# Kernel optimization log

Measured on AMD Instinct MI355X. Metric: run time of the kernel, lower is better.

Reference implementation:

```python
import jax, jax.numpy as jnp
import numpy as np
import math

IN_DIM = 512
OUT_DIM = 512
MOD_DIM = 512
B, S = 4, 4096
EPS = 1e-8


def setup_inputs() -> dict:
    key = jax.random.key(0)
    k1, k2, k3, k4 = jax.random.split(key, 4)
    x = jax.random.normal(k1, (B, S, IN_DIM), dtype=jnp.float32)
    modulation = jax.random.normal(k2, (B, S, MOD_DIM), dtype=jnp.float32)
    # main weight: kaiming_normal_(a=0.2, fan_in, leaky_relu) -> std = sqrt(2/(1+0.2^2)) / sqrt(in_dim)
    gain = math.sqrt(2.0 / (1.0 + 0.2 ** 2))
    weight = gain / math.sqrt(IN_DIM) * jax.random.normal(k3, (OUT_DIM, IN_DIM), dtype=jnp.float32)
    bias = jnp.zeros((OUT_DIM,), dtype=jnp.float32)
    # modulation Linear: cips_bias_init -> weight ~ N(0, 1/sqrt(fan_in)), bias = 1.0
    mod_w = (1.0 / math.sqrt(MOD_DIM)) * jax.random.normal(k4, (IN_DIM, MOD_DIM), dtype=jnp.float32)
    mod_b = jnp.ones((IN_DIM,), dtype=jnp.float32)
    return {"x": x, "modulation": modulation, "weight": weight, "bias": bias,
            "mod_w": mod_w, "mod_b": mod_b}


def reference(x, modulation, weight, bias, mod_w, mod_b):
    # s = modulation linear -> per-token scale on input features  [B,S,in]
    s = jnp.einsum('bsm,im->bsi', modulation, mod_w) + mod_b
    # Algebraic rewrite of StyleGAN2 modulated linear (same math, never
    # materializes [B,S,out,in]):
    #   out[b,s,o] = sum_i (W[o,i]*s[b,s,i]*demod[b,s,o]) * x[b,s,i]
    #             = demod[b,s,o] * sum_i W[o,i] * (s*x)[b,s,i]
    #   demod = rsqrt(sum_i (W[o,i]*s[b,s,i])^2 + eps)
    out = jnp.einsum('bsi,oi->bso', x * s, weight)
    demod = jax.lax.rsqrt(jnp.einsum('bsi,oi->bso', s * s, weight * weight) + EPS)
    # torch computes demod under no_grad -> constant; irrelevant for fwd but kept explicit
    out = out * jax.lax.stop_gradient(demod) + bias
    return out
```

## Files before the change

### kernel.cpp

```cpp
#include <hip/hip_runtime.h>
#include <hip/hip_bf16.h>


#define T_TOK 16384
#define DIM 512

typedef __attribute__((ext_vector_type(4))) float f32x4;
typedef __attribute__((ext_vector_type(8))) short bf16x8;

static __device__ __forceinline__ unsigned short f2bf(float f) {
    union { float f; unsigned int u; } v; v.f = f;
    unsigned int u = v.u;
    u += 0x7fffu + ((u >> 16) & 1u);
    return (unsigned short)(u >> 16);
}
static __device__ __forceinline__ float bf2f(unsigned short h) {
    union { unsigned int u; float f; } v; v.u = ((unsigned int)h) << 16;
    return v.f;
}

__global__ __launch_bounds__(256) void k0_convert(
    const float* __restrict__ mod, const float* __restrict__ weight,
    const float* __restrict__ mod_w,
    unsigned short* __restrict__ modb, unsigned short* __restrict__ Wb,
    unsigned short* __restrict__ W2b, unsigned short* __restrict__ mwb)
{
    const int NV_MOD = (T_TOK * DIM) / 4;
    const int NV_W   = (DIM * DIM) / 4;
    int idx = blockIdx.x * blockDim.x + threadIdx.x;
    int stride = gridDim.x * blockDim.x;
    for (int i = idx; i < NV_MOD; i += stride) {
        f32x4 v = ((const f32x4*)mod)[i];
        ushort4 o; o.x = f2bf(v[0]); o.y = f2bf(v[1]); o.z = f2bf(v[2]); o.w = f2bf(v[3]);
        ((ushort4*)modb)[i] = o;
    }
    for (int i = idx; i < NV_W; i += stride) {
        f32x4 v = ((const f32x4*)weight)[i];
        ushort4 o;  o.x = f2bf(v[0]); o.y = f2bf(v[1]); o.z = f2bf(v[2]); o.w = f2bf(v[3]);
        ((ushort4*)Wb)[i] = o;
        ushort4 o2; o2.x = f2bf(v[0]*v[0]); o2.y = f2bf(v[1]*v[1]);
                    o2.z = f2bf(v[2]*v[2]); o2.w = f2bf(v[3]*v[3]);
        ((ushort4*)W2b)[i] = o2;
        f32x4 m = ((const f32x4*)mod_w)[i];
        ushort4 o3; o3.x = f2bf(m[0]); o3.y = f2bf(m[1]); o3.z = f2bf(m[2]); o3.w = f2bf(m[3]);
        ((ushort4*)mwb)[i] = o3;
    }
}


__global__ __launch_bounds__(256, 2) void k1_style(
    const unsigned short* __restrict__ modb,
    const unsigned short* __restrict__ mwb,
    const float* __restrict__ x,
    const float* __restrict__ mod_b,
    unsigned short* __restrict__ xs,
    unsigned short* __restrict__ ss)
{
    __shared__ union {
        struct { unsigned short A[128 * 64]; unsigned short B[128 * 64]; } stg;
        unsigned short str[128 * 144];
    } u;
    const int tid  = threadIdx.x;
    const int lane = tid & 63;
    const int w    = tid >> 6;
    const int wr   = w >> 1, wc = w & 1;
    const int nbn  = DIM / 128;
    const int bm   = blockIdx.x / nbn;
    const int bn   = blockIdx.x % nbn;

    const int srow  = lane >> 3;
    const int lslot = (lane & 7) ^ srow;
    const int fr    = lane & 15;
    const int fs    = lane >> 4;

    f32x4 acc[4][4] = {};

    const size_t aBase = (size_t)bm * 128 * DIM;
    const size_t bBase = (size_t)bn * 128 * DIM;

    for (int kb = 0; kb < DIM; kb += 64) {
#pragma unroll
        for (int q = 0; q < 4; ++q) {
            int row = w * 32 + q * 8 + srow;
            const unsigned short* ga = modb + aBase + (size_t)row * DIM + kb + lslot * 8;
            const unsigned short* gb = mwb  + bBase + (size_t)row * DIM + kb + lslot * 8;
            __builtin_amdgcn_global_load_lds(
                (__attribute__((address_space(1))) void*)ga,
                (__attribute__((address_space(3))) void*)(u.stg.A + w * 2048 + q * 512), 16, 0, 0);
            __builtin_amdgcn_global_load_lds(
                (__attribute__((address_space(1))) void*)gb,
                (__attribute__((address_space(3))) void*)(u.stg.B + w * 2048 + q * 512), 16, 0, 0);
        }
        __syncthreads();
#pragma unroll
        for (int kk = 0; kk < 64; kk += 32) {
            bf16x8 af[4], bfv[4];
#pragma unroll
            for (int mi = 0; mi < 4; ++mi) {
                int row = wr * 64 + mi * 16 + fr;
                int ps  = ((kk >> 3) + fs) ^ (fr & 7);
                af[mi] = *(const bf16x8*)(u.stg.A + row * 64 + ps * 8);
            }
#pragma unroll
            for (int ni = 0; ni < 4; ++ni) {
                int row = wc * 64 + ni * 16 + fr;
                int ps  = ((kk >> 3) + fs) ^ (fr & 7);
                bfv[ni] = *(const bf16x8*)(u.stg.B + row * 64 + ps * 8);
            }
#pragma unroll
            for (int mi = 0; mi < 4; ++mi)
#pragma unroll
                for (int ni = 0; ni < 4; ++ni)
                    acc[mi][ni] = __builtin_amdgcn_mfma_f32_16x16x32_bf16(
                        af[mi], bfv[ni], acc[mi][ni], 0, 0, 0);
        }
        __syncthreads();
    }

#pragma unroll
    for (int ni = 0; ni < 4; ++ni) {
        int col = wc * 64 + ni * 16 + fr;
        float mb = mod_b[bn * 128 + col];
#pragma unroll
        for (int mi = 0; mi < 4; ++mi) {
#pragma unroll
            for (int j = 0; j < 4; ++j) {
                int row = wr * 64 + mi * 16 + fs * 4 + j;
                u.str[row * 144 + col] = f2bf(acc[mi][ni][j] + mb);
            }
        }
    }
    __syncthreads();
#pragma unroll
    for (int q = 0; q < 8; ++q) {
        int row = w * 32 + q * 4 + (lane >> 4);
        int c8  = (lane & 15) * 8;
        bf16x8 s8 = *(const bf16x8*)(u.str + row * 144 + c8);
        size_t off = ((size_t)bm * 128 + row) * DIM + bn * 128 + c8;
        f32x4 x0 = *(const f32x4*)(x + off);
        f32x4 x1 = *(const f32x4*)(x + off + 4);
        bf16x8 xsv, ssv;
#pragma unroll
        for (int e = 0; e < 8; ++e) {
            float sf = bf2f((unsigned short)s8[e]);
            float xv = (e < 4) ? x0[e] : x1[e - 4];
            xsv[e] = (short)f2bf(xv * sf);
            ssv[e] = (short)f2bf(sf * sf);
        }
        *(bf16x8*)(xs + off) = xsv;
        *(bf16x8*)(ss + off) = ssv;
    }
}

__global__ __launch_bounds__(256, 2) void k2_main(
    const unsigned short* __restrict__ xs,
    const unsigned short* __restrict__ ss,
    const unsigned short* __restrict__ Wb,
    const unsigned short* __restrict__ W2b,
    const float* __restrict__ bias,
    float* __restrict__ out)
{
    __shared__ unsigned short lXS[128 * 64];
    __shared__ unsigned short lSS[128 * 64];
    __shared__ unsigned short lW [128 * 64];
    __shared__ unsigned short lW2[128 * 64];
    const int tid  = threadIdx.x;
    const int lane = tid & 63;
    const int w    = tid >> 6;
    const int wr   = w >> 1, wc = w & 1;
    const int tile = (blockIdx.x & 7) * 64 + (blockIdx.x >> 3);
    const int bm   = tile >> 2;
    const int bn   = tile & 3;

    const int srow  = lane >> 3;
    const int lslot = (lane & 7) ^ srow;
    const int fr    = lane & 15;
    const int fs    = lane >> 4;

    f32x4 a1[4][4] = {};
    f32x4 a2[4][4] = {};

    const size_t aBase = (size_t)bm * 128 * DIM;
    const size_t bBase = (size_t)bn * 128 * DIM;

    for (int kb = 0; kb < DIM; kb += 64) {
#pragma unroll
        for (int q = 0; q < 4; ++q) {
            int row = w * 32 + q * 8 + srow;
            size_t goffA = aBase + (size_t)row * DIM + kb + lslot * 8;
            size_t goffB = bBase + (size_t)row * DIM + kb + lslot * 8;
            unsigned ldso = w * 2048 + q * 512;
            __builtin_amdgcn_global_load_lds(
                (__attribute__((address_space(1))) void*)(xs + goffA),
                (__attribute__((address_space(3))) void*)(lXS + ldso), 16, 0, 0);
            __builtin_amdgcn_global_load_lds(
                (__attribute__((address_space(1))) void*)(ss + goffA),
                (__attribute__((address_space(3))) void*)(lSS + ldso), 16, 0, 0);
            __builtin_amdgcn_global_load_lds(
                (__attribute__((address_space(1))) void*)(Wb + goffB),
                (__attribute__((address_space(3))) void*)(lW + ldso), 16, 0, 0);
            __builtin_amdgcn_global_load_lds(
                (__attribute__((address_space(1))) void*)(W2b + goffB),
                (__attribute__((address_space(3))) void*)(lW2 + ldso), 16, 0, 0);
        }
        __syncthreads();
#pragma unroll
        for (int kk = 0; kk < 64; kk += 32) {
            bf16x8 axs[4], ass[4], bw[4], bw2[4];
#pragma unroll
            for (int mi = 0; mi < 4; ++mi) {
                int row = wr * 64 + mi * 16 + fr;
                int ps  = ((kk >> 3) + fs) ^ (fr & 7);
                axs[mi] = *(const bf16x8*)(lXS + row * 64 + ps * 8);
                ass[mi] = *(const bf16x8*)(lSS + row * 64 + ps * 8);
            }
#pragma unroll
            for (int ni = 0; ni < 4; ++ni) {
                int row = wc * 64 + ni * 16 + fr;
                int ps  = ((kk >> 3) + fs) ^ (fr & 7);
                bw[ni]  = *(const bf16x8*)(lW  + row * 64 + ps * 8);
                bw2[ni] = *(const bf16x8*)(lW2 + row * 64 + ps * 8);
            }
#pragma unroll
            for (int mi = 0; mi < 4; ++mi)
#pragma unroll
                for (int ni = 0; ni < 4; ++ni) {
                    a1[mi][ni] = __builtin_amdgcn_mfma_f32_16x16x32_bf16(
                        axs[mi], bw[ni], a1[mi][ni], 0, 0, 0);
                    a2[mi][ni] = __builtin_amdgcn_mfma_f32_16x16x32_bf16(
                        ass[mi], bw2[ni], a2[mi][ni], 0, 0, 0);
                }
        }
        __syncthreads();
    }

#pragma unroll
    for (int ni = 0; ni < 4; ++ni) {
        int o = bn * 128 + wc * 64 + ni * 16 + fr;
        float bo = bias[o];
#pragma unroll
        for (int mi = 0; mi < 4; ++mi) {
#pragma unroll
            for (int j = 0; j < 4; ++j) {
                size_t t = (size_t)bm * 128 + wr * 64 + mi * 16 + fs * 4 + j;
                float d = rsqrtf(a2[mi][ni][j] + 1e-8f);
                out[t * DIM + o] = a1[mi][ni][j] * d + bo;
            }
        }
    }
}

extern "C" void kernel_launch(void* const* d_in, const int* in_sizes, int n_in,
                              void* d_out, int out_size, void* d_ws, size_t ws_size,
                              hipStream_t stream) {
    const float* x      = (const float*)d_in[0];
    const float* mod    = (const float*)d_in[1];
    const float* weight = (const float*)d_in[2];
    const float* bias   = (const float*)d_in[3];
    const float* mod_w  = (const float*)d_in[4];
    const float* mod_b  = (const float*)d_in[5];
    float* out = (float*)d_out;

    char* ws = (char*)d_ws;
    unsigned short* modb = (unsigned short*)(ws);
    unsigned short* xs   = (unsigned short*)(ws + (size_t)16777216);
    unsigned short* ssb  = (unsigned short*)(ws + (size_t)2 * 16777216);
    unsigned short* Wb   = (unsigned short*)(ws + (size_t)3 * 16777216);
    unsigned short* W2b  = (unsigned short*)(ws + (size_t)3 * 16777216 + 524288);
    unsigned short* mwb  = (unsigned short*)(ws + (size_t)3 * 16777216 + 2 * 524288);

    hipLaunchKernelGGL(k0_convert, dim3(2048), dim3(256), 0, stream,
                       mod, weight, mod_w, modb, Wb, W2b, mwb);
    hipLaunchKernelGGL(k1_style, dim3(512), dim3(256), 0, stream,
                       modb, mwb, x, mod_b, xs, ssb);
    hipLaunchKernelGGL(k2_main, dim3(512), dim3(256), 0, stream,
                       xs, ssb, Wb, W2b, bias, out);
}
```

Measured before the change: 54.79 us.

## Double-buffer k2 LDS staging with 32-wide K tiles and stage output through LDS

The main GEMM kernel now stages K in 32-wide slices across two LDS buffers, issuing the next slice's global-to-LDS loads before computing on the current one so load latency overlaps MFMA work. The epilogue writes results into an LDS transpose buffer (sharing space with the staging buffers through a union) and then stores 16-byte vectors per row, replacing scattered scalar stores. The cost is more barriers per K step, a new XOR swizzle scheme, and extra LDS traffic in the epilogue. LDS use grows to about 66KB, which may limit occupancy against the launch bound of 2 blocks per CU.

```diff
diff --git a/kernel.cpp b/kernel.cpp
--- a/kernel.cpp
+++ b/kernel.cpp
@@ -46,7 +46,6 @@
         ((ushort4*)mwb)[i] = o3;
     }
 }
-
 
 __global__ __launch_bounds__(256, 2) void k1_style(
     const unsigned short* __restrict__ modb,
@@ -160,10 +159,10 @@
     const float* __restrict__ bias,
     float* __restrict__ out)
 {
-    __shared__ unsigned short lXS[128 * 64];
-    __shared__ unsigned short lSS[128 * 64];
-    __shared__ unsigned short lW [128 * 64];
-    __shared__ unsigned short lW2[128 * 64];
+    __shared__ union {
+        unsigned short stg[2][4][128 * 32];
+        float tr[128 * 132];
+    } u;
     const int tid  = threadIdx.x;
     const int lane = tid & 63;
     const int w    = tid >> 6;
@@ -172,10 +171,8 @@
     const int bm   = tile >> 2;
     const int bn   = tile & 3;
 
-    const int srow  = lane >> 3;
-    const int lslot = (lane & 7) ^ srow;
-    const int fr    = lane & 15;
-    const int fs    = lane >> 4;
+    const int fr = lane & 15;
+    const int fs = lane >> 4;
 
     f32x4 a1[4][4] = {};
     f32x4 a2[4][4] = {};
@@ -183,70 +180,93 @@
     const size_t aBase = (size_t)bm * 128 * DIM;
     const size_t bBase = (size_t)bn * 128 * DIM;
 
-    for (int kb = 0; kb < DIM; kb += 64) {
-#pragma unroll
-        for (int q = 0; q < 4; ++q) {
-            int row = w * 32 + q * 8 + srow;
-            size_t goffA = aBase + (size_t)row * DIM + kb + lslot * 8;
-            size_t goffB = bBase + (size_t)row * DIM + kb + lslot * 8;
-            unsigned ldso = w * 2048 + q * 512;
-            __builtin_amdgcn_global_load_lds(
-                (__attribute__((address_space(1))) void*)(xs + goffA),
-                (__attribute__((address_space(3))) void*)(lXS + ldso), 16, 0, 0);
-            __builtin_amdgcn_global_load_lds(
-                (__attribute__((address_space(1))) void*)(ss + goffA),
-                (__attribute__((address_space(3))) void*)(lSS + ldso), 16, 0, 0);
-            __builtin_amdgcn_global_load_lds(
-                (__attribute__((address_space(1))) void*)(Wb + goffB),
-                (__attribute__((address_space(3))) void*)(lW + ldso), 16, 0, 0);
-            __builtin_amdgcn_global_load_lds(
-                (__attribute__((address_space(1))) void*)(W2b + goffB),
-                (__attribute__((address_space(3))) void*)(lW2 + ldso), 16, 0, 0);
-        }
-        __syncthreads();
-#pragma unroll
-        for (int kk = 0; kk < 64; kk += 32) {
-            bf16x8 axs[4], ass[4], bw[4], bw2[4];
-#pragma unroll
-            for (int mi = 0; mi < 4; ++mi) {
-                int row = wr * 64 + mi * 16 + fr;
-                int ps  = ((kk >> 3) + fs) ^ (fr & 7);
-                axs[mi] = *(const bf16x8*)(lXS + row * 64 + ps * 8);
-                ass[mi] = *(const bf16x8*)(lSS + row * 64 + ps * 8);
-            }
+    const int srw  = lane >> 2;
+    const int sp   = lane & 3;
+
+    auto STAGE = [&](int buf, int kb) {
+#pragma unroll
+        for (int q = 0; q < 2; ++q) {
+            int rb   = w * 32 + q * 16;
+            int row  = rb + srw;
+            int slog = sp ^ (row & 3);
+            size_t gA = aBase + (size_t)row * DIM + kb + slog * 8;
+            size_t gB = bBase + (size_t)row * DIM + kb + slog * 8;
+            __builtin_amdgcn_global_load_lds(
+                (__attribute__((address_space(1))) void*)(xs + gA),
+                (__attribute__((address_space(3))) void*)(u.stg[buf][0] + rb * 32), 16, 0, 0);
+            __builtin_amdgcn_global_load_lds(
+                (__attribute__((address_space(1))) void*)(ss + gA),
+                (__attribute__((address_space(3))) void*)(u.stg[buf][1] + rb * 32), 16, 0, 0);
+            __builtin_amdgcn_global_load_lds(
+                (__attribute__((address_space(1))) void*)(Wb + gB),
+                (__attribute__((address_space(3))) void*)(u.stg[buf][2] + rb * 32), 16, 0, 0);
+            __builtin_amdgcn_global_load_lds(
+                (__attribute__((address_space(1))) void*)(W2b + gB),
+                (__attribute__((address_space(3))) void*)(u.stg[buf][3] + rb * 32), 16, 0, 0);
+        }
+    };
+
+    auto COMPUTE = [&](int buf) {
+        bf16x8 axs[4], ass[4], bw[4], bw2[4];
+#pragma unroll
+        for (int mi = 0; mi < 4; ++mi) {
+            int row = wr * 64 + mi * 16 + fr;
+            int off = row * 32 + (fs ^ (row & 3)) * 8;
+            axs[mi] = *(const bf16x8*)(u.stg[buf][0] + off);
+            ass[mi] = *(const bf16x8*)(u.stg[buf][1] + off);
+        }
+#pragma unroll
+        for (int ni = 0; ni < 4; ++ni) {
+            int row = wc * 64 + ni * 16 + fr;
+            int off = row * 32 + (fs ^ (row & 3)) * 8;
+            bw[ni]  = *(const bf16x8*)(u.stg[buf][2] + off);
+            bw2[ni] = *(const bf16x8*)(u.stg[buf][3] + off);
+        }
+#pragma unroll
+        for (int mi = 0; mi < 4; ++mi)
 #pragma unroll
             for (int ni = 0; ni < 4; ++ni) {
-                int row = wc * 64 + ni * 16 + fr;
-                int ps  = ((kk >> 3) + fs) ^ (fr & 7);
-                bw[ni]  = *(const bf16x8*)(lW  + row * 64 + ps * 8);
-                bw2[ni] = *(const bf16x8*)(lW2 + row * 64 + ps * 8);
-            }
-#pragma unroll
-            for (int mi = 0; mi < 4; ++mi)
-#pragma unroll
-                for (int ni = 0; ni < 4; ++ni) {
-                    a1[mi][ni] = __builtin_amdgcn_mfma_f32_16x16x32_bf16(
-                        axs[mi], bw[ni], a1[mi][ni], 0, 0, 0);
-                    a2[mi][ni] = __builtin_amdgcn_mfma_f32_16x16x32_bf16(
-                        ass[mi], bw2[ni], a2[mi][ni], 0, 0, 0);
-                }
-        }
+                a1[mi][ni] = __builtin_amdgcn_mfma_f32_16x16x32_bf16(
+                    axs[mi], bw[ni], a1[mi][ni], 0, 0, 0);
+                a2[mi][ni] = __builtin_amdgcn_mfma_f32_16x16x32_bf16(
+                    ass[mi], bw2[ni], a2[mi][ni], 0, 0, 0);
+            }
+    };
+
+    STAGE(0, 0);
+    __syncthreads();
+#pragma unroll 1
+    for (int it = 0; it < 8; ++it) {
+        int kb0 = it * 64;
+        STAGE(1, kb0 + 32);
+        COMPUTE(0);
+        __syncthreads();
+        if (it < 7) STAGE(0, kb0 + 64);
+        COMPUTE(1);
         __syncthreads();
     }
 
 #pragma unroll
     for (int ni = 0; ni < 4; ++ni) {
-        int o = bn * 128 + wc * 64 + ni * 16 + fr;
-        float bo = bias[o];
+        int col = wc * 64 + ni * 16 + fr;
+        float bo = bias[bn * 128 + col];
 #pragma unroll
         for (int mi = 0; mi < 4; ++mi) {
 #pragma unroll
             for (int j = 0; j < 4; ++j) {
-                size_t t = (size_t)bm * 128 + wr * 64 + mi * 16 + fs * 4 + j;
+                int row = wr * 64 + mi * 16 + fs * 4 + j;
                 float d = rsqrtf(a2[mi][ni][j] + 1e-8f);
-                out[t * DIM + o] = a1[mi][ni][j] * d + bo;
-            }
-        }
+                u.tr[row * 132 + col] = a1[mi][ni][j] * d + bo;
+            }
+        }
+    }
+    __syncthreads();
+#pragma unroll
+    for (int i = 0; i < 16; ++i) {
+        int row  = w * 32 + i * 2 + (lane >> 5);
+        int colw = (lane & 31) * 4;
+        f32x4 v = *(const f32x4*)(u.tr + row * 132 + colw);
+        *(f32x4*)(out + ((size_t)bm * 128 + row) * DIM + bn * 128 + colw) = v;
     }
 }
 
```

New measurement: 75.93 us. +38.6%, slower.
